# Kernel tuning notes

Measured on AMD Instinct MI355X. Metric: run time of the kernel, lower is better.

Reference implementation:

```python
import jax, jax.numpy as jnp
import numpy as np

N, IN_DIM, OUT_DIM, HEADS = 8192, 256, 256, 2
C = OUT_DIM // HEADS  # per-head channel dim (concat=True)
ALPHA = 0.2
NEG = -9e15


def setup_inputs() -> dict:
    key = jax.random.key(0)
    ks = jax.random.split(key, 9)
    h = jax.random.normal(ks[0], (N, IN_DIM), dtype=jnp.float32)
    adj = jax.random.randint(ks[1], (N, N), 0, 2, dtype=jnp.int32)
    # torch nn.Linear weights are [out, in]; xavier-like scale
    def xav(k, shape):
        fan_in, fan_out = shape[1], shape[0]
        s = 1.414 * np.sqrt(6.0 / (fan_in + fan_out))
        return jax.random.uniform(k, shape, jnp.float32, -s, s)
    W1 = xav(ks[2], (HEADS * C, IN_DIM))
    W2 = xav(ks[3], (HEADS * C, IN_DIM))
    W3 = xav(ks[4], (HEADS * C, IN_DIM))
    b1 = jnp.zeros((HEADS * C,), jnp.float32)
    b2 = jnp.zeros((HEADS * C,), jnp.float32)
    b3 = jnp.zeros((HEADS * C,), jnp.float32)
    sa = 1.414 * np.sqrt(6.0 / (HEADS + 2 * C))
    a = jax.random.uniform(ks[5], (HEADS, 2 * C), jnp.float32, -sa, sa)
    return {"h": h, "adj": adj, "W1": W1, "b1": b1, "W2": W2, "b2": b2,
            "W3": W3, "b3": b3, "a": a}


def reference(h, adj, W1, b1, W2, b2, W3, b3, a):
    n = h.shape[0]
    W1h = (h @ W1.T + b1).reshape(n, HEADS, C)  # [N,H,C]
    W2h = (h @ W2.T + b2).reshape(n, HEADS, C)
    W3h = (h @ W3.T + b3).reshape(n, HEADS, C)
    # eij = a . [W1h_i || W2h_j] decomposes into per-node scores
    a1, a2 = a[:, :C], a[:, C:]
    s1 = jnp.einsum('nhc,hc->nh', W1h, a1)  # [N,H]
    s2 = jnp.einsum('nhc,hc->nh', W2h, a2)  # [N,H]
    e = jax.nn.leaky_relu(s1[:, None, :] + s2[None, :, :], ALPHA)  # [N,N,H]
    e = jnp.where(adj[:, :, None] == 1, e, NEG)
    att = jax.nn.softmax(e, axis=1)  # softmax over source dim j (dim=1)
    # dropout is identity in eval mode (training=False)
    h_prime = jnp.einsum('ijh,jhc->ihc', att, W3h)  # [N,H,C]
    return h_prime.reshape(n, HEADS * C)
```

## Files before the change

kernel.cpp:

```cpp
#include <hip/hip_runtime.h>
#include <hip/hip_bf16.h>

#define NN 8192
#define LOG2E 1.44269504088896f
#define S_SPLIT 8
#define JC 1024
#define NT 32

typedef __attribute__((ext_vector_type(8))) short short8;
typedef __attribute__((ext_vector_type(4))) float f32x4;

static __device__ __forceinline__ float bf2f(unsigned short u) {
    union { unsigned int i; float f; } v; v.i = ((unsigned int)u) << 16; return v.f;
}
static __device__ __forceinline__ unsigned short f2bf(float f) {
    union { float f; unsigned int i; } v; v.f = f;
    unsigned int lsb = (v.i >> 16) & 1u;
    v.i += 0x7fffu + lsb;
    return (unsigned short)(v.i >> 16);
}
static __device__ __forceinline__ unsigned int cvtpk(float lo, float hi) {
    unsigned int r;
    asm("v_cvt_pk_bf16_f32 %0, %1, %2" : "=v"(r) : "v"(lo), "v"(hi));
    return r;
}
static __device__ __forceinline__ float fexp2(float x) { return __builtin_amdgcn_exp2f(x); }

static __device__ __forceinline__ void cvt8(const float* __restrict__ p, short8& hi, short8& lo) {
    float4 u = *(const float4*)p;
    float4 v = *(const float4*)(p + 4);
    float f[8] = {u.x, u.y, u.z, u.w, v.x, v.y, v.z, v.w};
#pragma unroll
    for (int j = 0; j < 8; ++j) {
        unsigned short hb = f2bf(f[j]);
        hi[j] = (short)hb;
        lo[j] = (short)f2bf(f[j] - bf2f(hb));
    }
}

__global__ __launch_bounds__(256) void pack_kernel(const int* __restrict__ adj,
                                                   unsigned int* __restrict__ abits,
                                                   const float* __restrict__ W3,
                                                   unsigned short* __restrict__ w3hi,
                                                   unsigned short* __restrict__ w3lo) {
    int b = blockIdx.x;
    if (b < 8192) {
        int w = b * 256 + threadIdx.x;
        const int* src = adj + (size_t)w * 32;
        unsigned int bits = 0;
#pragma unroll
        for (int k = 0; k < 8; ++k) {
            int4 v = *(const int4*)(src + k * 4);
            bits |= (unsigned int)(v.x & 1) << (k * 4 + 0);
            bits |= (unsigned int)(v.y & 1) << (k * 4 + 1);
            bits |= (unsigned int)(v.z & 1) << (k * 4 + 2);
            bits |= (unsigned int)(v.w & 1) << (k * 4 + 3);
        }
        abits[w] = bits;
    } else {
        int i = (b - 8192) * 256 + threadIdx.x;
        float f = W3[i];
        unsigned short hb = f2bf(f);
        w3hi[i] = hb;
        w3lo[i] = f2bf(f - bf2f(hb));
    }
}

__global__ void prep_partial(const float* __restrict__ W1, const float* __restrict__ W2,
                             const float* __restrict__ a,
                             float* __restrict__ v1p, float* __restrict__ v2p) {
    int b = blockIdx.x;
    int t = threadIdx.x;
    int hh = t >> 8, k = t & 255;
    int c0 = (b & 7) * 16;
    const float* W = (b < 8) ? W1 : W2;
    int aoff = (b < 8) ? 0 : 128;
    float acc = 0.f;
    for (int c = c0; c < c0 + 16; ++c)
        acc += W[(size_t)(hh * 128 + c) * 256 + k] * a[hh * 256 + aoff + c];
    ((b < 8) ? v1p : v2p)[(b & 7) * 512 + t] = acc;
}

__global__ void prep_reduce(const float* __restrict__ b1, const float* __restrict__ b2,
                            const float* __restrict__ a,
                            const float* __restrict__ v1p, const float* __restrict__ v2p,
                            float* __restrict__ v1, float* __restrict__ v2, float* __restrict__ bd) {
    int t = threadIdx.x;
    float a1 = 0.f, a2 = 0.f;
    for (int b = 0; b < 8; ++b) { a1 += v1p[b * 512 + t]; a2 += v2p[b * 512 + t]; }
    v1[t] = a1;
    v2[t] = a2;
    int g = t >> 7;
    int hh = g >> 1, which = g & 1, c = t & 127;
    float prod = which ? b2[hh * 128 + c] * a[hh * 256 + 128 + c]
                       : b1[hh * 128 + c] * a[hh * 256 + c];
#pragma unroll
    for (int off = 1; off < 64; off <<= 1) prod += __shfl_xor(prod, off);
    __shared__ float ws[8];
    if ((t & 63) == 0) ws[t >> 6] = prod;
    __syncthreads();
    if (t < 4) bd[t] = ws[2 * t] + ws[2 * t + 1];
}

__global__ __launch_bounds__(256) void s_kernel(const float* __restrict__ hmat,
                         const float* __restrict__ v1, const float* __restrict__ v2,
                         const float* __restrict__ bd,
                         float* __restrict__ s1o, float* __restrict__ s2o) {
    int w = threadIdx.x >> 6, l = threadIdx.x & 63;
    int n = blockIdx.x * 4 + w;
    float4 hv  = *(const float4*)(hmat + (size_t)n * 256 + l * 4);
    float4 va0 = *(const float4*)(v1 + l * 4);
    float4 va1 = *(const float4*)(v1 + 256 + l * 4);
    float4 vb0 = *(const float4*)(v2 + l * 4);
    float4 vb1 = *(const float4*)(v2 + 256 + l * 4);
    float s10 = hv.x*va0.x + hv.y*va0.y + hv.z*va0.z + hv.w*va0.w;
    float s11 = hv.x*va1.x + hv.y*va1.y + hv.z*va1.z + hv.w*va1.w;
    float s20 = hv.x*vb0.x + hv.y*vb0.y + hv.z*vb0.z + hv.w*vb0.w;
    float s21 = hv.x*vb1.x + hv.y*vb1.y + hv.z*vb1.z + hv.w*vb1.w;
#pragma unroll
    for (int off = 1; off < 64; off <<= 1) {
        s10 += __shfl_xor(s10, off);
        s11 += __shfl_xor(s11, off);
        s20 += __shfl_xor(s20, off);
        s21 += __shfl_xor(s21, off);
    }
    if (l == 0) {
        s1o[n*2 + 0] = (s10 + bd[0]) * LOG2E;
        s1o[n*2 + 1] = (s11 + bd[2]) * LOG2E;
        s2o[n]       = (s20 + bd[1]) * LOG2E;
        s2o[NN + n]  = (s21 + bd[3]) * LOG2E;
    }
}

__global__ __launch_bounds__(256) void w3_kernel(const float* __restrict__ hmat,
                                                 const unsigned short* __restrict__ w3hi,
                                                 const unsigned short* __restrict__ w3lo,
                                                 const float* __restrict__ b3,
                                                 unsigned short* __restrict__ w3b) {
    int tid = threadIdx.x;
    int w = tid >> 6, l = tid & 63;
    int m = l & 15, kq = l >> 4;
    int n0 = (blockIdx.x * 2 + (w & 1)) * 16;
    int c0 = (w >> 1) * 8;
    f32x4 acc[8];
#pragma unroll
    for (int ct = 0; ct < 8; ++ct) acc[ct] = (f32x4){0.f, 0.f, 0.f, 0.f};
    for (int k0 = 0; k0 < 256; k0 += 32) {
        short8 ahi, alo;
        cvt8(hmat + (size_t)(n0 + m) * 256 + k0 + kq * 8, ahi, alo);
#pragma unroll
        for (int ct = 0; ct < 8; ++ct) {
            int c = (c0 + ct) * 16 + m;
            short8 bhi = *(const short8*)&w3hi[(size_t)c * 256 + k0 + kq * 8];
            short8 blo = *(const short8*)&w3lo[(size_t)c * 256 + k0 + kq * 8];
            acc[ct] = __builtin_amdgcn_mfma_f32_16x16x32_bf16(ahi, bhi, acc[ct], 0, 0, 0);
            acc[ct] = __builtin_amdgcn_mfma_f32_16x16x32_bf16(alo, bhi, acc[ct], 0, 0, 0);
            acc[ct] = __builtin_amdgcn_mfma_f32_16x16x32_bf16(ahi, blo, acc[ct], 0, 0, 0);
        }
    }
#pragma unroll
    for (int ct = 0; ct < 8; ++ct) {
        int c = (c0 + ct) * 16 + m;
        float bias = b3[c];
#pragma unroll
        for (int e = 0; e < 4; ++e) {
            int n = n0 + kq * 4 + e;
            size_t idx = ((size_t)(n >> 5) * 16 + (c >> 4)) * 512 + (size_t)((((n >> 3) & 3) * 16 + m) * 8 + (n & 7));
            w3b[idx] = f2bf(acc[ct][e] + bias);
        }
    }
}

__global__ __launch_bounds__(256, 4) void attn_fused(
        const unsigned int* __restrict__ abits, const float* __restrict__ s1a,
        const float* __restrict__ s2h, const unsigned short* __restrict__ w3b,
        unsigned short* __restrict__ pacc, float* __restrict__ pden)
{
    __shared__ unsigned short Pt[2][2][64][32];
    __shared__ float s2t[2][JC];
    __shared__ unsigned int abt[64][32];

    const int tid = threadIdx.x;
    const int ln = tid & 63;
    const int m = ln & 15, kq = ln >> 4;
    const int cg = tid >> 6;
    const int hw = cg >> 1;
    const int r = tid >> 2, oc = tid & 3;
    const int i0 = blockIdx.x * 64;
    const int sidx = blockIdx.y;
    const int j0 = sidx * JC;
    const int sw = kq ^ ((m >> 1) & 3);

    const float s1r0 = s1a[(i0 + r) * 2 + 0];
    const float s1r1 = s1a[(i0 + r) * 2 + 1];
    unsigned short* ptw = &Pt[0][0][0][0] + r * 32 + ((oc ^ ((r >> 1) & 3)) << 3);
    const unsigned short* pta = &Pt[0][0][0][0] + hw * 2048 + m * 32 + (sw << 3);
    const unsigned short* w3p = w3b + ((size_t)(j0 >> 5) * 16 + cg * 4) * 512 + ln * 8;

    f32x4 acc[4][4];
#pragma unroll
    for (int rt = 0; rt < 4; ++rt)
#pragma unroll
        for (int f = 0; f < 4; ++f) acc[rt][f] = (f32x4){0.f, 0.f, 0.f, 0.f};
    float d0 = 0.f, d1 = 0.f;

    for (int x = tid; x < 2 * JC; x += 256) {
        int h = x >> 10, j = x & (JC - 1);
        s2t[h][j] = s2h[(size_t)h * NN + j0 + j];
    }
    for (int x = tid; x < 64 * 32; x += 256) {
        int rr = x >> 5, tt = x & 31;
        abt[rr][tt] = abits[(size_t)(i0 + rr) * 256 + (j0 >> 5) + tt];
    }
    __syncthreads();

    for (int t = 0; t < NT; ++t) {
        const int buf = t & 1;
        const unsigned short* bp = w3p + (size_t)t * 8192;
        short8 bf0 = *(const short8*)(bp);
        short8 bf1 = *(const short8*)(bp + 512);
        short8 bf2 = *(const short8*)(bp + 1024);
        short8 bf3 = *(const short8*)(bp + 1536);
        {
            unsigned int bits = abt[r][t] >> (oc * 8);
            uint4 w0, w1;
            {
                float4 sv0 = *(const float4*)&s2t[0][t * 32 + oc * 8];
                float4 sv1 = *(const float4*)&s2t[1][t * 32 + oc * 8];
                float x0, q0, q1, q2, q3, u0, u1, u2, u3;
                x0 = s1r0 + sv0.x; x0 = fmaxf(x0, 0.2f * x0); q0 = (bits & 1u) ? fexp2(x0) : 0.f;
                x0 = s1r0 + sv0.y; x0 = fmaxf(x0, 0.2f * x0); q1 = (bits & 2u) ? fexp2(x0) : 0.f;
                x0 = s1r0 + sv0.z; x0 = fmaxf(x0, 0.2f * x0); q2 = (bits & 4u) ? fexp2(x0) : 0.f;
                x0 = s1r0 + sv0.w; x0 = fmaxf(x0, 0.2f * x0); q3 = (bits & 8u) ? fexp2(x0) : 0.f;
                x0 = s1r1 + sv1.x; x0 = fmaxf(x0, 0.2f * x0); u0 = (bits & 1u) ? fexp2(x0) : 0.f;
                x0 = s1r1 + sv1.y; x0 = fmaxf(x0, 0.2f * x0); u1 = (bits & 2u) ? fexp2(x0) : 0.f;
                x0 = s1r1 + sv1.z; x0 = fmaxf(x0, 0.2f * x0); u2 = (bits & 4u) ? fexp2(x0) : 0.f;
                x0 = s1r1 + sv1.w; x0 = fmaxf(x0, 0.2f * x0); u3 = (bits & 8u) ? fexp2(x0) : 0.f;
                d0 += (q0 + q1) + (q2 + q3);
                d1 += (u0 + u1) + (u2 + u3);
                w0.x = cvtpk(q0, q1); w0.y = cvtpk(q2, q3);
                w1.x = cvtpk(u0, u1); w1.y = cvtpk(u2, u3);
            }
            {
                float4 sv0 = *(const float4*)&s2t[0][t * 32 + oc * 8 + 4];
                float4 sv1 = *(const float4*)&s2t[1][t * 32 + oc * 8 + 4];
                float x0, q0, q1, q2, q3, u0, u1, u2, u3;
                x0 = s1r0 + sv0.x; x0 = fmaxf(x0, 0.2f * x0); q0 = (bits & 16u)  ? fexp2(x0) : 0.f;
                x0 = s1r0 + sv0.y; x0 = fmaxf(x0, 0.2f * x0); q1 = (bits & 32u)  ? fexp2(x0) : 0.f;
                x0 = s1r0 + sv0.z; x0 = fmaxf(x0, 0.2f * x0); q2 = (bits & 64u)  ? fexp2(x0) : 0.f;
                x0 = s1r0 + sv0.w; x0 = fmaxf(x0, 0.2f * x0); q3 = (bits & 128u) ? fexp2(x0) : 0.f;
                x0 = s1r1 + sv1.x; x0 = fmaxf(x0, 0.2f * x0); u0 = (bits & 16u)  ? fexp2(x0) : 0.f;
                x0 = s1r1 + sv1.y; x0 = fmaxf(x0, 0.2f * x0); u1 = (bits & 32u)  ? fexp2(x0) : 0.f;
                x0 = s1r1 + sv1.z; x0 = fmaxf(x0, 0.2f * x0); u2 = (bits & 64u)  ? fexp2(x0) : 0.f;
                x0 = s1r1 + sv1.w; x0 = fmaxf(x0, 0.2f * x0); u3 = (bits & 128u) ? fexp2(x0) : 0.f;
                d0 += (q0 + q1) + (q2 + q3);
                d1 += (u0 + u1) + (u2 + u3);
                w0.z = cvtpk(q0, q1); w0.w = cvtpk(q2, q3);
                w1.z = cvtpk(u0, u1); w1.w = cvtpk(u2, u3);
            }
            unsigned short* pw = ptw + buf * 4096;
            *(uint4*)pw = w0;
            *(uint4*)(pw + 2048) = w1;
        }
        asm volatile("s_waitcnt lgkmcnt(0)" ::: "memory");
        __builtin_amdgcn_sched_barrier(0);
        __builtin_amdgcn_s_barrier();
        asm volatile("" ::: "memory");
        {
            const unsigned short* pa = pta + buf * 4096;
            __builtin_amdgcn_s_setprio(1);
#pragma unroll
            for (int rt = 0; rt < 4; ++rt) {
                short8 a = *(const short8*)(pa + rt * 512);
                acc[rt][0] = __builtin_amdgcn_mfma_f32_16x16x32_bf16(a, bf0, acc[rt][0], 0, 0, 0);
                acc[rt][1] = __builtin_amdgcn_mfma_f32_16x16x32_bf16(a, bf1, acc[rt][1], 0, 0, 0);
                acc[rt][2] = __builtin_amdgcn_mfma_f32_16x16x32_bf16(a, bf2, acc[rt][2], 0, 0, 0);
                acc[rt][3] = __builtin_amdgcn_mfma_f32_16x16x32_bf16(a, bf3, acc[rt][3], 0, 0, 0);
            }
            __builtin_amdgcn_s_setprio(0);
        }
    }

    d0 += __shfl_xor(d0, 1); d0 += __shfl_xor(d0, 2);
    d1 += __shfl_xor(d1, 1); d1 += __shfl_xor(d1, 2);
    if (oc == 0) {
        size_t base = ((size_t)sidx * NN + i0 + r) * 2;
        pden[base + 0] = d0;
        pden[base + 1] = d1;
    }
    size_t pb_ = (size_t)sidx * NN * 256;
#pragma unroll
    for (int rt = 0; rt < 4; ++rt)
#pragma unroll
        for (int e = 0; e < 4; ++e) {
            int row = i0 + rt * 16 + kq * 4 + e;
#pragma unroll
            for (int f = 0; f < 4; ++f) {
                int col = cg * 64 + f * 16 + m;
                __builtin_nontemporal_store(f2bf(acc[rt][f][e]), &pacc[pb_ + (size_t)row * 256 + col]);
            }
        }
}

__global__ void combine_kernel(const unsigned short* __restrict__ pacc, const float* __restrict__ pden,
                               float* __restrict__ out) {
    size_t idx = ((size_t)blockIdx.x * 256 + threadIdx.x) * 8;
    int i = (int)(idx >> 8);
    int c = (int)(idx & 255);
    int hh = c >> 7;
    float acc[8];
#pragma unroll
    for (int e = 0; e < 8; ++e) acc[e] = 0.f;
    float den = 0.f;
    for (int s = 0; s < S_SPLIT; ++s) {
        uint4 v = *(const uint4*)&pacc[(size_t)s * NN * 256 + idx];
        unsigned int uu[4] = {v.x, v.y, v.z, v.w};
#pragma unroll
        for (int q = 0; q < 4; ++q) {
            acc[2*q]   += bf2f((unsigned short)(uu[q] & 0xffff));
            acc[2*q+1] += bf2f((unsigned short)(uu[q] >> 16));
        }
        den += pden[((size_t)s * NN + i) * 2 + hh];
    }
    float r = 1.f / den;
    float4 o0 = {acc[0]*r, acc[1]*r, acc[2]*r, acc[3]*r};
    float4 o1 = {acc[4]*r, acc[5]*r, acc[6]*r, acc[7]*r};
    *(float4*)&out[idx] = o0;
    *(float4*)&out[idx + 4] = o1;
}

extern "C" void kernel_launch(void* const* d_in, const int* in_sizes, int n_in,
                              void* d_out, int out_size, void* d_ws, size_t ws_size,
                              hipStream_t stream) {
    const float* hmat = (const float*)d_in[0];
    const int*   adj  = (const int*)d_in[1];
    const float* W1   = (const float*)d_in[2];
    const float* b1   = (const float*)d_in[3];
    const float* W2   = (const float*)d_in[4];
    const float* b2   = (const float*)d_in[5];
    const float* W3   = (const float*)d_in[6];
    const float* b3   = (const float*)d_in[7];
    const float* a    = (const float*)d_in[8];
    float* out = (float*)d_out;

    char* p = (char*)d_ws;
    float* v1   = (float*)p; p += 2048;
    float* v2   = (float*)p; p += 2048;
    float* bd   = (float*)p; p += 256;
    float* s1   = (float*)p; p += (size_t)NN * 2 * sizeof(float);
    float* s2h  = (float*)p; p += (size_t)NN * 2 * sizeof(float);
    float* v1p  = (float*)p; p += 8 * 512 * sizeof(float);
    float* v2p  = (float*)p; p += 8 * 512 * sizeof(float);
    unsigned short* w3hi = (unsigned short*)p; p += 65536 * 2;
    unsigned short* w3lo = (unsigned short*)p; p += 65536 * 2;
    unsigned short* w3b  = (unsigned short*)p; p += (size_t)NN * 256 * 2;
    unsigned int* abits  = (unsigned int*)p;   p += (size_t)NN * 256 * sizeof(unsigned int);
    float* pden = (float*)p; p += (size_t)S_SPLIT * NN * 2 * sizeof(float);
    unsigned short* pacc = (unsigned short*)p;

    pack_kernel<<<8192 + 256, 256, 0, stream>>>(adj, abits, W3, w3hi, w3lo);
    prep_partial<<<16, 512, 0, stream>>>(W1, W2, a, v1p, v2p);
    prep_reduce<<<1, 512, 0, stream>>>(b1, b2, a, v1p, v2p, v1, v2, bd);
    s_kernel<<<NN / 4, 256, 0, stream>>>(hmat, v1, v2, bd, s1, s2h);
    w3_kernel<<<256, 256, 0, stream>>>(hmat, w3hi, w3lo, b3, w3b);
    attn_fused<<<dim3(NN / 64, S_SPLIT), 256, 0, stream>>>(abits, s1, s2h, w3b, pacc, pden);
    combine_kernel<<<(NN * 256) / (256 * 8), 256, 0, stream>>>(pacc, pden, out);
}
```

Before: 152.0 us.

## Fuse adjacency bit-packing into attention kernel via async LDS prefetch

Removes the separate pack kernel that compressed the int32 adjacency into bitmasks. The attention kernel now streams raw int32 adjacency tiles straight into shared memory with global_load_lds, double-buffered one tile ahead. The W3 hi/lo split moves into extra blocks of s_kernel. This drops one kernel launch and the write and re-read of the bitmask array, but each attention block now reads the full int32 adjacency tile and waits on vmcnt every iteration.

```diff
diff --git a/kernel.cpp b/kernel.cpp
--- a/kernel.cpp
+++ b/kernel.cpp
@@ -35,34 +35,6 @@
         unsigned short hb = f2bf(f[j]);
         hi[j] = (short)hb;
         lo[j] = (short)f2bf(f[j] - bf2f(hb));
-    }
-}
-
-__global__ __launch_bounds__(256) void pack_kernel(const int* __restrict__ adj,
-                                                   unsigned int* __restrict__ abits,
-                                                   const float* __restrict__ W3,
-                                                   unsigned short* __restrict__ w3hi,
-                                                   unsigned short* __restrict__ w3lo) {
-    int b = blockIdx.x;
-    if (b < 8192) {
-        int w = b * 256 + threadIdx.x;
-        const int* src = adj + (size_t)w * 32;
-        unsigned int bits = 0;
-#pragma unroll
-        for (int k = 0; k < 8; ++k) {
-            int4 v = *(const int4*)(src + k * 4);
-            bits |= (unsigned int)(v.x & 1) << (k * 4 + 0);
-            bits |= (unsigned int)(v.y & 1) << (k * 4 + 1);
-            bits |= (unsigned int)(v.z & 1) << (k * 4 + 2);
-            bits |= (unsigned int)(v.w & 1) << (k * 4 + 3);
-        }
-        abits[w] = bits;
-    } else {
-        int i = (b - 8192) * 256 + threadIdx.x;
-        float f = W3[i];
-        unsigned short hb = f2bf(f);
-        w3hi[i] = hb;
-        w3lo[i] = f2bf(f - bf2f(hb));
     }
 }
 
@@ -105,7 +77,17 @@
 __global__ __launch_bounds__(256) void s_kernel(const float* __restrict__ hmat,
                          const float* __restrict__ v1, const float* __restrict__ v2,
                          const float* __restrict__ bd,
-                         float* __restrict__ s1o, float* __restrict__ s2o) {
+                         float* __restrict__ s1o, float* __restrict__ s2o,
+                         const float* __restrict__ W3,
+                         unsigned short* __restrict__ w3hi, unsigned short* __restrict__ w3lo) {
+    if (blockIdx.x >= NN / 4) {
+        int i = (blockIdx.x - NN / 4) * 256 + threadIdx.x;
+        float f = W3[i];
+        unsigned short hb = f2bf(f);
+        w3hi[i] = hb;
+        w3lo[i] = f2bf(f - bf2f(hb));
+        return;
+    }
     int w = threadIdx.x >> 6, l = threadIdx.x & 63;
     int n = blockIdx.x * 4 + w;
     float4 hv  = *(const float4*)(hmat + (size_t)n * 256 + l * 4);
@@ -172,13 +154,13 @@
 }
 
 __global__ __launch_bounds__(256, 4) void attn_fused(
-        const unsigned int* __restrict__ abits, const float* __restrict__ s1a,
+        const int* __restrict__ adj, const float* __restrict__ s1a,
         const float* __restrict__ s2h, const unsigned short* __restrict__ w3b,
         unsigned short* __restrict__ pacc, float* __restrict__ pden)
 {
     __shared__ unsigned short Pt[2][2][64][32];
     __shared__ float s2t[2][JC];
-    __shared__ unsigned int abt[64][32];
+    __shared__ int adjt[2][64][32];
 
     const int tid = threadIdx.x;
     const int ln = tid & 63;
@@ -197,6 +179,18 @@
     const unsigned short* pta = &Pt[0][0][0][0] + hw * 2048 + m * 32 + (sw << 3);
     const unsigned short* w3p = w3b + ((size_t)(j0 >> 5) * 16 + cg * 4) * 512 + ln * 8;
 
+    auto stageAdj = [&](int bsel, int jt) {
+#pragma unroll
+        for (int it = 0; it < 2; ++it) {
+            int g = it * 256 + tid;
+            const int* src = adj + (size_t)(i0 + (g >> 3)) * NN + j0 + jt + (g & 7) * 4;
+            __builtin_amdgcn_global_load_lds(
+                (const __attribute__((address_space(1))) void*)src,
+                (__attribute__((address_space(3))) void*)((char*)&adjt[bsel][0][0] + g * 16),
+                16, 0, 0);
+        }
+    };
+
     f32x4 acc[4][4];
 #pragma unroll
     for (int rt = 0; rt < 4; ++rt)
@@ -208,34 +202,34 @@
         int h = x >> 10, j = x & (JC - 1);
         s2t[h][j] = s2h[(size_t)h * NN + j0 + j];
     }
-    for (int x = tid; x < 64 * 32; x += 256) {
-        int rr = x >> 5, tt = x & 31;
-        abt[rr][tt] = abits[(size_t)(i0 + rr) * 256 + (j0 >> 5) + tt];
-    }
+    stageAdj(0, 0);
+    asm volatile("s_waitcnt vmcnt(0)" ::: "memory");
     __syncthreads();
 
     for (int t = 0; t < NT; ++t) {
         const int buf = t & 1;
+        if (t + 1 < NT) stageAdj(buf ^ 1, (t + 1) * 32);
         const unsigned short* bp = w3p + (size_t)t * 8192;
         short8 bf0 = *(const short8*)(bp);
         short8 bf1 = *(const short8*)(bp + 512);
         short8 bf2 = *(const short8*)(bp + 1024);
         short8 bf3 = *(const short8*)(bp + 1536);
         {
-            unsigned int bits = abt[r][t] >> (oc * 8);
+            int4 A0 = *(const int4*)&adjt[buf][r][oc * 8];
+            int4 A1 = *(const int4*)&adjt[buf][r][oc * 8 + 4];
             uint4 w0, w1;
             {
                 float4 sv0 = *(const float4*)&s2t[0][t * 32 + oc * 8];
                 float4 sv1 = *(const float4*)&s2t[1][t * 32 + oc * 8];
                 float x0, q0, q1, q2, q3, u0, u1, u2, u3;
-                x0 = s1r0 + sv0.x; x0 = fmaxf(x0, 0.2f * x0); q0 = (bits & 1u) ? fexp2(x0) : 0.f;
-                x0 = s1r0 + sv0.y; x0 = fmaxf(x0, 0.2f * x0); q1 = (bits & 2u) ? fexp2(x0) : 0.f;
-                x0 = s1r0 + sv0.z; x0 = fmaxf(x0, 0.2f * x0); q2 = (bits & 4u) ? fexp2(x0) : 0.f;
-                x0 = s1r0 + sv0.w; x0 = fmaxf(x0, 0.2f * x0); q3 = (bits & 8u) ? fexp2(x0) : 0.f;
-                x0 = s1r1 + sv1.x; x0 = fmaxf(x0, 0.2f * x0); u0 = (bits & 1u) ? fexp2(x0) : 0.f;
-                x0 = s1r1 + sv1.y; x0 = fmaxf(x0, 0.2f * x0); u1 = (bits & 2u) ? fexp2(x0) : 0.f;
-                x0 = s1r1 + sv1.z; x0 = fmaxf(x0, 0.2f * x0); u2 = (bits & 4u) ? fexp2(x0) : 0.f;
-                x0 = s1r1 + sv1.w; x0 = fmaxf(x0, 0.2f * x0); u3 = (bits & 8u) ? fexp2(x0) : 0.f;
+                x0 = s1r0 + sv0.x; x0 = fmaxf(x0, 0.2f * x0); q0 = A0.x ? fexp2(x0) : 0.f;
+                x0 = s1r0 + sv0.y; x0 = fmaxf(x0, 0.2f * x0); q1 = A0.y ? fexp2(x0) : 0.f;
+                x0 = s1r0 + sv0.z; x0 = fmaxf(x0, 0.2f * x0); q2 = A0.z ? fexp2(x0) : 0.f;
+                x0 = s1r0 + sv0.w; x0 = fmaxf(x0, 0.2f * x0); q3 = A0.w ? fexp2(x0) : 0.f;
+                x0 = s1r1 + sv1.x; x0 = fmaxf(x0, 0.2f * x0); u0 = A0.x ? fexp2(x0) : 0.f;
+                x0 = s1r1 + sv1.y; x0 = fmaxf(x0, 0.2f * x0); u1 = A0.y ? fexp2(x0) : 0.f;
+                x0 = s1r1 + sv1.z; x0 = fmaxf(x0, 0.2f * x0); u2 = A0.z ? fexp2(x0) : 0.f;
+                x0 = s1r1 + sv1.w; x0 = fmaxf(x0, 0.2f * x0); u3 = A0.w ? fexp2(x0) : 0.f;
                 d0 += (q0 + q1) + (q2 + q3);
                 d1 += (u0 + u1) + (u2 + u3);
                 w0.x = cvtpk(q0, q1); w0.y = cvtpk(q2, q3);
@@ -245,14 +239,14 @@
                 float4 sv0 = *(const float4*)&s2t[0][t * 32 + oc * 8 + 4];
                 float4 sv1 = *(const float4*)&s2t[1][t * 32 + oc * 8 + 4];
                 float x0, q0, q1, q2, q3, u0, u1, u2, u3;
-                x0 = s1r0 + sv0.x; x0 = fmaxf(x0, 0.2f * x0); q0 = (bits & 16u)  ? fexp2(x0) : 0.f;
-                x0 = s1r0 + sv0.y; x0 = fmaxf(x0, 0.2f * x0); q1 = (bits & 32u)  ? fexp2(x0) : 0.f;
-                x0 = s1r0 + sv0.z; x0 = fmaxf(x0, 0.2f * x0); q2 = (bits & 64u)  ? fexp2(x0) : 0.f;
-                x0 = s1r0 + sv0.w; x0 = fmaxf(x0, 0.2f * x0); q3 = (bits & 128u) ? fexp2(x0) : 0.f;
-                x0 = s1r1 + sv1.x; x0 = fmaxf(x0, 0.2f * x0); u0 = (bits & 16u)  ? fexp2(x0) : 0.f;
-                x0 = s1r1 + sv1.y; x0 = fmaxf(x0, 0.2f * x0); u1 = (bits & 32u)  ? fexp2(x0) : 0.f;
-                x0 = s1r1 + sv1.z; x0 = fmaxf(x0, 0.2f * x0); u2 = (bits & 64u)  ? fexp2(x0) : 0.f;
-                x0 = s1r1 + sv1.w; x0 = fmaxf(x0, 0.2f * x0); u3 = (bits & 128u) ? fexp2(x0) : 0.f;
+                x0 = s1r0 + sv0.x; x0 = fmaxf(x0, 0.2f * x0); q0 = A1.x ? fexp2(x0) : 0.f;
+                x0 = s1r0 + sv0.y; x0 = fmaxf(x0, 0.2f * x0); q1 = A1.y ? fexp2(x0) : 0.f;
+                x0 = s1r0 + sv0.z; x0 = fmaxf(x0, 0.2f * x0); q2 = A1.z ? fexp2(x0) : 0.f;
+                x0 = s1r0 + sv0.w; x0 = fmaxf(x0, 0.2f * x0); q3 = A1.w ? fexp2(x0) : 0.f;
+                x0 = s1r1 + sv1.x; x0 = fmaxf(x0, 0.2f * x0); u0 = A1.x ? fexp2(x0) : 0.f;
+                x0 = s1r1 + sv1.y; x0 = fmaxf(x0, 0.2f * x0); u1 = A1.y ? fexp2(x0) : 0.f;
+                x0 = s1r1 + sv1.z; x0 = fmaxf(x0, 0.2f * x0); u2 = A1.z ? fexp2(x0) : 0.f;
+                x0 = s1r1 + sv1.w; x0 = fmaxf(x0, 0.2f * x0); u3 = A1.w ? fexp2(x0) : 0.f;
                 d0 += (q0 + q1) + (q2 + q3);
                 d1 += (u0 + u1) + (u2 + u3);
                 w0.z = cvtpk(q0, q1); w0.w = cvtpk(q2, q3);
@@ -262,7 +256,7 @@
             *(uint4*)pw = w0;
             *(uint4*)(pw + 2048) = w1;
         }
-        asm volatile("s_waitcnt lgkmcnt(0)" ::: "memory");
+        asm volatile("s_waitcnt vmcnt(0) lgkmcnt(0)" ::: "memory");
         __builtin_amdgcn_sched_barrier(0);
         __builtin_amdgcn_s_barrier();
         asm volatile("" ::: "memory");
@@ -354,15 +348,13 @@
     unsigned short* w3hi = (unsigned short*)p; p += 65536 * 2;
     unsigned short* w3lo = (unsigned short*)p; p += 65536 * 2;
     unsigned short* w3b  = (unsigned short*)p; p += (size_t)NN * 256 * 2;
-    unsigned int* abits  = (unsigned int*)p;   p += (size_t)NN * 256 * sizeof(unsigned int);
     float* pden = (float*)p; p += (size_t)S_SPLIT * NN * 2 * sizeof(float);
     unsigned short* pacc = (unsigned short*)p;
 
-    pack_kernel<<<8192 + 256, 256, 0, stream>>>(adj, abits, W3, w3hi, w3lo);
     prep_partial<<<16, 512, 0, stream>>>(W1, W2, a, v1p, v2p);
     prep_reduce<<<1, 512, 0, stream>>>(b1, b2, a, v1p, v2p, v1, v2, bd);
-    s_kernel<<<NN / 4, 256, 0, stream>>>(hmat, v1, v2, bd, s1, s2h);
+    s_kernel<<<NN / 4 + 256, 256, 0, stream>>>(hmat, v1, v2, bd, s1, s2h, W3, w3hi, w3lo);
     w3_kernel<<<256, 256, 0, stream>>>(hmat, w3hi, w3lo, b3, w3b);
-    attn_fused<<<dim3(NN / 64, S_SPLIT), 256, 0, stream>>>(abits, s1, s2h, w3b, pacc, pden);
+    attn_fused<<<dim3(NN / 64, S_SPLIT), 256, 0, stream>>>(adj, s1, s2h, w3b, pacc, pden);
     combine_kernel<<<(NN * 256) / (256 * 8), 256, 0, stream>>>(pacc, pden, out);
 }
```

Result: slower. 156.4 us (+2.9%).
